# Kernel optimization log

Hardware: AMD Instinct MI355X
Metric: run time of the kernel (lower is better)

## Reference

```python
import math
import jax, jax.numpy as jnp
import numpy as np

B, S, D, H = 2, 2048, 2048, 16  # batch, seq, d_model, n_heads


def setup_inputs() -> dict:
    key = jax.random.key(0)
    ks = jax.random.split(key, 5)
    w_scale = 1.0 / math.sqrt(D)
    return {
        "x": jax.random.normal(ks[0], (B, S, D), jnp.float32),
        "attn_bias": jax.random.normal(ks[1], (1, H, S, S), jnp.float32) * 0.1,
        "Wqkv_w": jax.random.normal(ks[2], (3 * D, D), jnp.float32) * w_scale,
        "Wqkv_b": jnp.zeros((3 * D,), jnp.float32),
        "out_w": jax.random.normal(ks[3], (D, D), jnp.float32) * w_scale,
        "out_b": jnp.zeros((D,), jnp.float32),
    }


def reference(x, attn_bias, Wqkv_w, Wqkv_b, out_w, out_b):
    b, s, d = x.shape
    hd = d // H                      # head dim = 128
    scale = 1.0 / math.sqrt(hd)      # module default: 1/sqrt(d_model // n_heads)

    # fused QKV projection
    qkv = x @ Wqkv_w.T + Wqkv_b                       # [b, s, 3d]
    q, k, v = jnp.split(qkv, 3, axis=2)               # each [b, s, d]
    q = q.reshape(b, s, H, hd).transpose(0, 2, 1, 3)  # [b, h, s, hd]
    k = k.reshape(b, s, H, hd).transpose(0, 2, 1, 3)
    v = v.reshape(b, s, H, hd).transpose(0, 2, 1, 3)

    # scaled scores + additive bias (bias sliced to trailing q/k lengths)
    scores = jnp.einsum('bhqd,bhkd->bhqk', q, k) * scale
    scores = scores + attn_bias[:, :, -s:, -s:]

    # causal mask, masked positions set to dtype min (matches masked_fill with finfo.min)
    causal = jnp.tril(jnp.ones((s, s), dtype=bool))   # True = keep
    min_val = jnp.finfo(scores.dtype).min
    scores = jnp.where(causal[None, None, :, :], scores, min_val)

    p = jax.nn.softmax(scores, axis=-1)               # [b, h, s, s]
    out = jnp.einsum('bhqk,bhkd->bhqd', p, v)         # [b, h, s, hd]
    out = out.transpose(0, 2, 1, 3).reshape(b, s, d)  # [b, s, d]

    return out @ out_w.T + out_b
```

## Files before the change

kernel.cpp:

```cpp
#include <hip/hip_runtime.h>
#include <hip/hip_bf16.h>
#include <stdint.h>

#define H_  16
#define S_  2048
#define D_  2048
#define HD_ 128

typedef __bf16 bf16x8 __attribute__((ext_vector_type(8)));
typedef short  s16x8  __attribute__((ext_vector_type(8)));
typedef float  f32x4  __attribute__((ext_vector_type(4)));
typedef unsigned short u16x4 __attribute__((ext_vector_type(4)));

__device__ __forceinline__ unsigned short f2bf(float f) {
    unsigned u = __builtin_bit_cast(unsigned, f);
    u += 0x7fffu + ((u >> 16) & 1u);
    return (unsigned short)(u >> 16);
}

__device__ __forceinline__ float bf2f(unsigned short u) {
    unsigned v = ((unsigned)u) << 16;
    return __builtin_bit_cast(float, v);
}

__device__ __forceinline__ bf16x8 ld_bf8(const unsigned short* p) {
    s16x8 r = *reinterpret_cast<const s16x8*>(p);
    return __builtin_bit_cast(bf16x8, r);
}

#define GLOAD_LDS16(gp, lp)                                                     \
    __builtin_amdgcn_global_load_lds(                                            \
        (const __attribute__((address_space(1))) void*)(gp),                     \
        (__attribute__((address_space(3))) void*)(lp), 16, 0, 0)

__global__ __launch_bounds__(256) void cast_f32_bf16(const float* __restrict__ in,
                                                     unsigned short* __restrict__ out,
                                                     int n) {
    int i = (blockIdx.x * 256 + threadIdx.x) * 4;
    if (i >= n) return;
    float4 v = *reinterpret_cast<const float4*>(in + i);
    u16x4 o;
    o[0] = f2bf(v.x); o[1] = f2bf(v.y); o[2] = f2bf(v.z); o[3] = f2bf(v.w);
    *reinterpret_cast<u16x4*>(out + i) = o;
}

__global__ __launch_bounds__(256) void gemm_bt_qkv(const unsigned short* __restrict__ A,
                                                   const unsigned short* __restrict__ W,
                                                   const float* __restrict__ bias,
                                                   unsigned short* __restrict__ Qo,
                                                   unsigned short* __restrict__ Ko,
                                                   unsigned short* __restrict__ Vo) {
    __shared__ alignas(16) unsigned short As[128 * 32];
    __shared__ alignas(16) unsigned short Bs[128 * 32];
    const int t  = threadIdx.x;
    const int l  = t & 63, w = t >> 6;
    const int wr = w >> 1, wc = w & 1;
    const int lr = l & 15, g = l >> 4;

    const int GX = 48, NWG = 1536, CPX = NWG / 8;
    const int raw = blockIdx.y * GX + blockIdx.x;
    const int swz = (raw & 7) * CPX + (raw >> 3);
    const int m0 = (swz / GX) * 128, n0 = (swz % GX) * 128;
    const int Kd = D_;

    f32x4 zero = {0.f, 0.f, 0.f, 0.f};
    f32x4 acc[4][4];
    for (int i = 0; i < 4; ++i)
        for (int j = 0; j < 4; ++j) acc[i][j] = zero;

    const int ea = t * 8;
    const int rowA = ea >> 5, colA = ea & 31;

    for (int kt = 0; kt < Kd; kt += 32) {
        GLOAD_LDS16(A + (size_t)(m0 + rowA) * Kd + kt + colA, &As[ea]);
        GLOAD_LDS16(A + (size_t)(m0 + 64 + rowA) * Kd + kt + colA, &As[2048 + ea]);
        GLOAD_LDS16(W + (size_t)(n0 + rowA) * Kd + kt + colA, &Bs[ea]);
        GLOAD_LDS16(W + (size_t)(n0 + 64 + rowA) * Kd + kt + colA, &Bs[2048 + ea]);
        __syncthreads();
        bf16x8 af[4], bfr[4];
        for (int mi = 0; mi < 4; ++mi) af[mi]  = ld_bf8(&As[(wr * 64 + mi * 16 + lr) * 32 + g * 8]);
        for (int ni = 0; ni < 4; ++ni) bfr[ni] = ld_bf8(&Bs[(wc * 64 + ni * 16 + lr) * 32 + g * 8]);
        for (int mi = 0; mi < 4; ++mi)
            for (int ni = 0; ni < 4; ++ni)
                acc[mi][ni] = __builtin_amdgcn_mfma_f32_16x16x32_bf16(af[mi], bfr[ni], acc[mi][ni], 0, 0, 0);
        __syncthreads();
    }

    for (int mi = 0; mi < 4; ++mi) {
        for (int ni = 0; ni < 4; ++ni) {
            for (int i = 0; i < 4; ++i) {
                int m = m0 + wr * 64 + mi * 16 + g * 4 + i;
                int n = n0 + wc * 64 + ni * 16 + lr;
                float v = acc[mi][ni][i] + bias[n];
                int which = n >> 11;
                int n2 = n & 2047;
                int h = n2 >> 7, d = n2 & 127;
                int b = m >> 11, s = m & 2047;
                size_t idx = (((size_t)(b * H_ + h)) * S_ + s) * HD_ + d;
                unsigned short bv = f2bf(v);
                if (which == 0)      Qo[idx] = bv;
                else if (which == 1) Ko[idx] = bv;
                else                 Vo[idx] = bv;
            }
        }
    }
}

__global__ void transpose_v(const unsigned short* __restrict__ V,
                            unsigned short* __restrict__ Vt) {
    __shared__ alignas(16) unsigned short tile[32][33];
    const int bh = blockIdx.z;
    const int d0 = blockIdx.x * 32, s0 = blockIdx.y * 32;
    const int tx = threadIdx.x, ty = threadIdx.y;
    for (int r = 0; r < 4; ++r) {
        int s = s0 + ty + r * 8;
        tile[ty + r * 8][tx] = V[((size_t)bh * S_ + s) * HD_ + d0 + tx];
    }
    __syncthreads();
    for (int r = 0; r < 4; ++r) {
        int d = d0 + ty + r * 8;
        Vt[((size_t)bh * HD_ + d) * S_ + s0 + tx] = tile[tx][ty + r * 8];
    }
}

__global__ __launch_bounds__(256) void attn_kernel8(const unsigned short* __restrict__ Q,
                                                    const unsigned short* __restrict__ K,
                                                    const unsigned short* __restrict__ Vt,
                                                    const float* __restrict__ biasPtr,
                                                    unsigned short* __restrict__ O) {
    __shared__ alignas(16) unsigned short Klds[2][8192];
    __shared__ alignas(16) unsigned short Vlds[2][8192];
    __shared__ alignas(16) unsigned short Pbuf[4][16 * 64];

    const int t  = threadIdx.x;
    const int l  = t & 63, w = t >> 6;
    const int lr = l & 15, g = l >> 4;

    const int raw   = blockIdx.x;
    const int xcd   = raw & 7;
    const int local = raw >> 3;
    const int cu    = local & 31;
    const int slot  = local >> 5;
    const int qt    = (slot & 1) ? cu : (31 - cu);
    const int bh    = xcd + 8 * slot;
    const int b     = bh >> 4, head = bh & 15;

    const unsigned short* Qb = Q + (size_t)bh * S_ * HD_;
    const unsigned short* Kb = K + (size_t)bh * S_ * HD_;
    const unsigned short* Vb = Vt + (size_t)bh * HD_ * S_;
    const float* Bh32 = biasPtr + (size_t)head * S_ * S_;
    const float scale = 0.08838834764831845f;

    const int q0 = qt * 64 + w * 16;

    bf16x8 qf[4];
#pragma unroll
    for (int dc = 0; dc < 4; ++dc)
        qf[dc] = ld_bf8(Qb + (size_t)(q0 + lr) * HD_ + dc * 32 + g * 8);

    f32x4 zero = {0.f, 0.f, 0.f, 0.f};
    f32x4 o[8];
#pragma unroll
    for (int nc = 0; nc < 8; ++nc) o[nc] = zero;
    float lp[4] = {0.f, 0.f, 0.f, 0.f};

    unsigned short* Pw = Pbuf[w];

    auto STAGE = [&](int buf, int k0) {
#pragma unroll
        for (int p = 0; p < 4; ++p) {
            int lin = p * 4096 + t * 16;
            int row = lin >> 8;
            int colb = lin & 255;
            int scolb = colb ^ ((row & 7) << 4);
            GLOAD_LDS16(Kb + (size_t)(k0 + row) * HD_ + (scolb >> 1), &Klds[buf][lin >> 1]);
        }
#pragma unroll
        for (int p = 0; p < 4; ++p) {
            int lin = p * 4096 + t * 16;
            int row = lin >> 7;
            int colb = lin & 127;
            int scolb = colb ^ ((row & 7) << 4);
            GLOAD_LDS16(Vb + (size_t)row * S_ + k0 + (scolb >> 1), &Vlds[buf][lin >> 1]);
        }
    };

    STAGE(0, 0);
    __syncthreads();

    int cur = 0;
    for (int c = 0; c <= qt; ++c) {
        const int k0 = c * 64;

        if (c < qt) STAGE(cur ^ 1, k0 + 64);

        float bias_r[4][4];
#pragma unroll
        for (int i = 0; i < 4; ++i) {
            const int boff = (q0 + g * 4 + i) * S_ + k0 + lr;
#pragma unroll
            for (int kc = 0; kc < 4; ++kc)
                bias_r[i][kc] = Bh32[boff + kc * 16];
        }

        f32x4 s[4];
#pragma unroll
        for (int kc = 0; kc < 4; ++kc) s[kc] = zero;
#pragma unroll
        for (int kc = 0; kc < 4; ++kc) {
            bf16x8 kf[4];
#pragma unroll
            for (int dc = 0; dc < 4; ++dc)
                kf[dc] = ld_bf8(&Klds[cur][(kc * 16 + lr) * 128 + ((dc * 32 + g * 8) ^ ((lr & 7) << 3))]);
#pragma unroll
            for (int dc = 0; dc < 4; ++dc)
                s[kc] = __builtin_amdgcn_mfma_f32_16x16x32_bf16(qf[dc], kf[dc], s[kc], 0, 0, 0);
        }

        const bool lastc = (c == qt);
#pragma unroll
        for (int i = 0; i < 4; ++i) {
            const int rl   = w * 16 + g * 4 + i;
            const int prow = g * 4 + i;
            float e[4];
#pragma unroll
            for (int kc = 0; kc < 4; ++kc) {
                float v = s[kc][i] * scale + bias_r[i][kc];
                if (lastc && (kc * 16 + lr > rl)) v = -1.0e30f;
                e[kc] = __expf(v - 16.0f);
            }
            lp[i] += (e[0] + e[1]) + (e[2] + e[3]);
            const int sw = (prow & 7) << 3;
            Pw[(prow * 64 + 0  + lr) ^ sw] = f2bf(e[0]);
            Pw[(prow * 64 + 16 + lr) ^ sw] = f2bf(e[1]);
            Pw[(prow * 64 + 32 + lr) ^ sw] = f2bf(e[2]);
            Pw[(prow * 64 + 48 + lr) ^ sw] = f2bf(e[3]);
        }

#pragma unroll
        for (int kc2 = 0; kc2 < 2; ++kc2) {
            bf16x8 pa = ld_bf8(&Pw[(lr * 64 + kc2 * 32 + g * 8) ^ ((lr & 7) << 3)]);
#pragma unroll
            for (int nc = 0; nc < 8; ++nc) {
                bf16x8 vf = ld_bf8(&Vlds[cur][(nc * 16 + lr) * 64 + ((kc2 * 32 + g * 8) ^ ((lr & 7) << 3))]);
                o[nc] = __builtin_amdgcn_mfma_f32_16x16x32_bf16(pa, vf, o[nc], 0, 0, 0);
            }
        }

        __syncthreads();
        cur ^= 1;
    }

#pragma unroll
    for (int i = 0; i < 4; ++i) {
        lp[i] += __shfl_xor(lp[i], 1);
        lp[i] += __shfl_xor(lp[i], 2);
        lp[i] += __shfl_xor(lp[i], 4);
        lp[i] += __shfl_xor(lp[i], 8);
    }

#pragma unroll
    for (int i = 0; i < 4; ++i) {
        float inv = 1.0f / lp[i];
        int row = q0 + g * 4 + i;
#pragma unroll
        for (int nc = 0; nc < 8; ++nc) {
            O[((size_t)(b * S_ + row)) * D_ + head * HD_ + nc * 16 + lr] = f2bf(o[nc][i] * inv);
        }
    }
}

__global__ __launch_bounds__(256) void gemm_bt_out(const unsigned short* __restrict__ A,
                                                   const unsigned short* __restrict__ W,
                                                   const float* __restrict__ bias,
                                                   float* __restrict__ out) {
    __shared__ alignas(16) unsigned short As[128 * 32];
    __shared__ alignas(16) unsigned short Bs[128 * 32];
    const int t  = threadIdx.x;
    const int l  = t & 63, w = t >> 6;
    const int wr = w >> 1, wc = w & 1;
    const int lr = l & 15, g = l >> 4;

    const int GX = 16, NWG = 512, CPX = NWG / 8;
    const int raw = blockIdx.y * GX + blockIdx.x;
    const int swz = (raw & 7) * CPX + (raw >> 3);
    const int m0 = (swz / GX) * 128, n0 = (swz % GX) * 128;
    const int Kd = D_;

    f32x4 zero = {0.f, 0.f, 0.f, 0.f};
    f32x4 acc[4][4];
    for (int i = 0; i < 4; ++i)
        for (int j = 0; j < 4; ++j) acc[i][j] = zero;

    const int ea = t * 8;
    const int rowA = ea >> 5, colA = ea & 31;

    for (int kt = 0; kt < Kd; kt += 32) {
        GLOAD_LDS16(A + (size_t)(m0 + rowA) * Kd + kt + colA, &As[ea]);
        GLOAD_LDS16(A + (size_t)(m0 + 64 + rowA) * Kd + kt + colA, &As[2048 + ea]);
        GLOAD_LDS16(W + (size_t)(n0 + rowA) * Kd + kt + colA, &Bs[ea]);
        GLOAD_LDS16(W + (size_t)(n0 + 64 + rowA) * Kd + kt + colA, &Bs[2048 + ea]);
        __syncthreads();
        bf16x8 af[4], bfr[4];
        for (int mi = 0; mi < 4; ++mi) af[mi]  = ld_bf8(&As[(wr * 64 + mi * 16 + lr) * 32 + g * 8]);
        for (int ni = 0; ni < 4; ++ni) bfr[ni] = ld_bf8(&Bs[(wc * 64 + ni * 16 + lr) * 32 + g * 8]);
        for (int mi = 0; mi < 4; ++mi)
            for (int ni = 0; ni < 4; ++ni)
                acc[mi][ni] = __builtin_amdgcn_mfma_f32_16x16x32_bf16(af[mi], bfr[ni], acc[mi][ni], 0, 0, 0);
        __syncthreads();
    }

    for (int mi = 0; mi < 4; ++mi) {
        for (int ni = 0; ni < 4; ++ni) {
            for (int i = 0; i < 4; ++i) {
                int m = m0 + wr * 64 + mi * 16 + g * 4 + i;
                int n = n0 + wc * 64 + ni * 16 + lr;
                out[(size_t)m * D_ + n] = acc[mi][ni][i] + bias[n];
            }
        }
    }
}

extern "C" void kernel_launch(void* const* d_in, const int* in_sizes, int n_in,
                              void* d_out, int out_size, void* d_ws, size_t ws_size,
                              hipStream_t stream) {
    (void)in_sizes; (void)n_in; (void)out_size; (void)ws_size;
    const float* x         = (const float*)d_in[0];
    const float* attn_bias = (const float*)d_in[1];
    const float* Wqkv_w    = (const float*)d_in[2];
    const float* Wqkv_b    = (const float*)d_in[3];
    const float* out_w     = (const float*)d_in[4];
    const float* out_b     = (const float*)d_in[5];
    float* out = (float*)d_out;

    char* ws = (char*)d_ws;
    unsigned short* xb    = (unsigned short*)(ws);
    unsigned short* wqkvb = (unsigned short*)(ws + 16777216);
    unsigned short* woutb = (unsigned short*)(ws + 41943040);
    unsigned short* Qb    = (unsigned short*)(ws + 50331648);
    unsigned short* Kb    = (unsigned short*)(ws + 67108864);
    unsigned short* Vb    = (unsigned short*)(ws + 83886080);
    unsigned short* Vtb   = wqkvb;
    unsigned short* Ob    = xb;

    cast_f32_bf16<<<8192, 256, 0, stream>>>(x, xb, 8388608);
    cast_f32_bf16<<<12288, 256, 0, stream>>>(Wqkv_w, wqkvb, 12582912);
    cast_f32_bf16<<<4096, 256, 0, stream>>>(out_w, woutb, 4194304);
    gemm_bt_qkv<<<dim3(48, 32), 256, 0, stream>>>(xb, wqkvb, Wqkv_b, Qb, Kb, Vb);
    transpose_v<<<dim3(4, 64, 32), dim3(32, 8), 0, stream>>>(Vb, Vtb);
    attn_kernel8<<<1024, 256, 0, stream>>>(Qb, Kb, Vtb, attn_bias, Ob);
    gemm_bt_out<<<dim3(16, 32), 256, 0, stream>>>(Ob, woutb, out_b, out);
}
```

Measured before the change: 329.8 us.

## Double attention query tile per wave and write V transposed from QKV GEMM

The attention kernel now handles 128 query rows per block (32 per wave, two 16-row MFMA tiles), so each staged K/V chunk in LDS serves twice as many queries, and the grid drops to 512 blocks. The QKV GEMM epilogue writes V directly in head-dim-major layout, which removes the separate transpose kernel and its launch. The cost is more accumulator registers, which may lower occupancy, and fewer blocks for load balancing across causal tiles. The V stores become strided, so the GEMM epilogue writes are less coalesced.

```diff
diff --git a/kernel.cpp b/kernel.cpp
--- a/kernel.cpp
+++ b/kernel.cpp
@@ -16,11 +16,6 @@
     unsigned u = __builtin_bit_cast(unsigned, f);
     u += 0x7fffu + ((u >> 16) & 1u);
     return (unsigned short)(u >> 16);
-}
-
-__device__ __forceinline__ float bf2f(unsigned short u) {
-    unsigned v = ((unsigned)u) << 16;
-    return __builtin_bit_cast(float, v);
 }
 
 __device__ __forceinline__ bf16x8 ld_bf8(const unsigned short* p) {
@@ -96,41 +91,26 @@
                 int n2 = n & 2047;
                 int h = n2 >> 7, d = n2 & 127;
                 int b = m >> 11, s = m & 2047;
-                size_t idx = (((size_t)(b * H_ + h)) * S_ + s) * HD_ + d;
                 unsigned short bv = f2bf(v);
-                if (which == 0)      Qo[idx] = bv;
-                else if (which == 1) Ko[idx] = bv;
-                else                 Vo[idx] = bv;
-            }
-        }
-    }
-}
-
-__global__ void transpose_v(const unsigned short* __restrict__ V,
-                            unsigned short* __restrict__ Vt) {
-    __shared__ alignas(16) unsigned short tile[32][33];
-    const int bh = blockIdx.z;
-    const int d0 = blockIdx.x * 32, s0 = blockIdx.y * 32;
-    const int tx = threadIdx.x, ty = threadIdx.y;
-    for (int r = 0; r < 4; ++r) {
-        int s = s0 + ty + r * 8;
-        tile[ty + r * 8][tx] = V[((size_t)bh * S_ + s) * HD_ + d0 + tx];
-    }
-    __syncthreads();
-    for (int r = 0; r < 4; ++r) {
-        int d = d0 + ty + r * 8;
-        Vt[((size_t)bh * HD_ + d) * S_ + s0 + tx] = tile[tx][ty + r * 8];
-    }
-}
-
-__global__ __launch_bounds__(256) void attn_kernel8(const unsigned short* __restrict__ Q,
+                if (which == 0)
+                    Qo[(((size_t)(b * H_ + h)) * S_ + s) * HD_ + d] = bv;
+                else if (which == 1)
+                    Ko[(((size_t)(b * H_ + h)) * S_ + s) * HD_ + d] = bv;
+                else
+                    Vo[(((size_t)(b * H_ + h)) * HD_ + d) * S_ + s] = bv;
+            }
+        }
+    }
+}
+
+__global__ __launch_bounds__(256) void attn_kernel9(const unsigned short* __restrict__ Q,
                                                     const unsigned short* __restrict__ K,
                                                     const unsigned short* __restrict__ Vt,
                                                     const float* __restrict__ biasPtr,
                                                     unsigned short* __restrict__ O) {
     __shared__ alignas(16) unsigned short Klds[2][8192];
     __shared__ alignas(16) unsigned short Vlds[2][8192];
-    __shared__ alignas(16) unsigned short Pbuf[4][16 * 64];
+    __shared__ alignas(16) unsigned short Pbuf[4][32 * 64];
 
     const int t  = threadIdx.x;
     const int l  = t & 63, w = t >> 6;
@@ -139,10 +119,10 @@
     const int raw   = blockIdx.x;
     const int xcd   = raw & 7;
     const int local = raw >> 3;
+    const int group = local >> 5;
     const int cu    = local & 31;
-    const int slot  = local >> 5;
-    const int qt    = (slot & 1) ? cu : (31 - cu);
-    const int bh    = xcd + 8 * slot;
+    const int qt    = group ? (cu & 15) : (15 - (cu & 15));
+    const int bh    = xcd + 8 * ((cu >> 4) + 2 * group);
     const int b     = bh >> 4, head = bh & 15;
 
     const unsigned short* Qb = Q + (size_t)bh * S_ * HD_;
@@ -151,18 +131,20 @@
     const float* Bh32 = biasPtr + (size_t)head * S_ * S_;
     const float scale = 0.08838834764831845f;
 
-    const int q0 = qt * 64 + w * 16;
-
-    bf16x8 qf[4];
-#pragma unroll
-    for (int dc = 0; dc < 4; ++dc)
-        qf[dc] = ld_bf8(Qb + (size_t)(q0 + lr) * HD_ + dc * 32 + g * 8);
+    const int q0 = qt * 128 + w * 32;
+
+    bf16x8 qf[2][4];
+#pragma unroll
+    for (int m = 0; m < 2; ++m)
+#pragma unroll
+        for (int dc = 0; dc < 4; ++dc)
+            qf[m][dc] = ld_bf8(Qb + (size_t)(q0 + m * 16 + lr) * HD_ + dc * 32 + g * 8);
 
     f32x4 zero = {0.f, 0.f, 0.f, 0.f};
-    f32x4 o[8];
-#pragma unroll
-    for (int nc = 0; nc < 8; ++nc) o[nc] = zero;
-    float lp[4] = {0.f, 0.f, 0.f, 0.f};
+    f32x4 o0[8], o1[8];
+#pragma unroll
+    for (int nc = 0; nc < 8; ++nc) { o0[nc] = zero; o1[nc] = zero; }
+    float lp[2][4] = {{0.f, 0.f, 0.f, 0.f}, {0.f, 0.f, 0.f, 0.f}};
 
     unsigned short* Pw = Pbuf[w];
 
@@ -188,24 +170,27 @@
     STAGE(0, 0);
     __syncthreads();
 
+    const int nch = 2 * qt + 2;
     int cur = 0;
-    for (int c = 0; c <= qt; ++c) {
+    for (int c = 0; c < nch; ++c) {
         const int k0 = c * 64;
 
-        if (c < qt) STAGE(cur ^ 1, k0 + 64);
-
-        float bias_r[4][4];
-#pragma unroll
-        for (int i = 0; i < 4; ++i) {
-            const int boff = (q0 + g * 4 + i) * S_ + k0 + lr;
-#pragma unroll
-            for (int kc = 0; kc < 4; ++kc)
-                bias_r[i][kc] = Bh32[boff + kc * 16];
-        }
-
-        f32x4 s[4];
-#pragma unroll
-        for (int kc = 0; kc < 4; ++kc) s[kc] = zero;
+        if (c + 1 < nch) STAGE(cur ^ 1, k0 + 64);
+
+        float bias_r[2][4][4];
+#pragma unroll
+        for (int m = 0; m < 2; ++m)
+#pragma unroll
+            for (int i = 0; i < 4; ++i) {
+                const int boff = (q0 + m * 16 + g * 4 + i) * S_ + k0 + lr;
+#pragma unroll
+                for (int kc = 0; kc < 4; ++kc)
+                    bias_r[m][i][kc] = Bh32[boff + kc * 16];
+            }
+
+        f32x4 s0[4], s1[4];
+#pragma unroll
+        for (int kc = 0; kc < 4; ++kc) { s0[kc] = zero; s1[kc] = zero; }
 #pragma unroll
         for (int kc = 0; kc < 4; ++kc) {
             bf16x8 kf[4];
@@ -213,37 +198,45 @@
             for (int dc = 0; dc < 4; ++dc)
                 kf[dc] = ld_bf8(&Klds[cur][(kc * 16 + lr) * 128 + ((dc * 32 + g * 8) ^ ((lr & 7) << 3))]);
 #pragma unroll
-            for (int dc = 0; dc < 4; ++dc)
-                s[kc] = __builtin_amdgcn_mfma_f32_16x16x32_bf16(qf[dc], kf[dc], s[kc], 0, 0, 0);
-        }
-
-        const bool lastc = (c == qt);
-#pragma unroll
-        for (int i = 0; i < 4; ++i) {
-            const int rl   = w * 16 + g * 4 + i;
-            const int prow = g * 4 + i;
-            float e[4];
-#pragma unroll
-            for (int kc = 0; kc < 4; ++kc) {
-                float v = s[kc][i] * scale + bias_r[i][kc];
-                if (lastc && (kc * 16 + lr > rl)) v = -1.0e30f;
-                e[kc] = __expf(v - 16.0f);
-            }
-            lp[i] += (e[0] + e[1]) + (e[2] + e[3]);
-            const int sw = (prow & 7) << 3;
-            Pw[(prow * 64 + 0  + lr) ^ sw] = f2bf(e[0]);
-            Pw[(prow * 64 + 16 + lr) ^ sw] = f2bf(e[1]);
-            Pw[(prow * 64 + 32 + lr) ^ sw] = f2bf(e[2]);
-            Pw[(prow * 64 + 48 + lr) ^ sw] = f2bf(e[3]);
+            for (int dc = 0; dc < 4; ++dc) {
+                s0[kc] = __builtin_amdgcn_mfma_f32_16x16x32_bf16(qf[0][dc], kf[dc], s0[kc], 0, 0, 0);
+                s1[kc] = __builtin_amdgcn_mfma_f32_16x16x32_bf16(qf[1][dc], kf[dc], s1[kc], 0, 0, 0);
+            }
+        }
+
+        const bool maskzone = (c >= nch - 2);
+#pragma unroll
+        for (int m = 0; m < 2; ++m) {
+#pragma unroll
+            for (int i = 0; i < 4; ++i) {
+                const int rowabs = q0 + m * 16 + g * 4 + i;
+                const int prow   = m * 16 + g * 4 + i;
+                float e[4];
+#pragma unroll
+                for (int kc = 0; kc < 4; ++kc) {
+                    float sv = (m == 0) ? s0[kc][i] : s1[kc][i];
+                    float v = sv * scale + bias_r[m][i][kc];
+                    if (maskzone && (k0 + kc * 16 + lr > rowabs)) v = -1.0e30f;
+                    e[kc] = __expf(v - 16.0f);
+                }
+                lp[m][i] += (e[0] + e[1]) + (e[2] + e[3]);
+                const int sw = (prow & 7) << 3;
+                Pw[(prow * 64 + 0  + lr) ^ sw] = f2bf(e[0]);
+                Pw[(prow * 64 + 16 + lr) ^ sw] = f2bf(e[1]);
+                Pw[(prow * 64 + 32 + lr) ^ sw] = f2bf(e[2]);
+                Pw[(prow * 64 + 48 + lr) ^ sw] = f2bf(e[3]);
+            }
         }
 
 #pragma unroll
         for (int kc2 = 0; kc2 < 2; ++kc2) {
-            bf16x8 pa = ld_bf8(&Pw[(lr * 64 + kc2 * 32 + g * 8) ^ ((lr & 7) << 3)]);
+            bf16x8 pa0 = ld_bf8(&Pw[((lr)      * 64 + ((kc2 * 32 + g * 8) ^ ((lr & 7) << 3)))]);
+            bf16x8 pa1 = ld_bf8(&Pw[((16 + lr) * 64 + ((kc2 * 32 + g * 8) ^ ((lr & 7) << 3)))]);
 #pragma unroll
             for (int nc = 0; nc < 8; ++nc) {
                 bf16x8 vf = ld_bf8(&Vlds[cur][(nc * 16 + lr) * 64 + ((kc2 * 32 + g * 8) ^ ((lr & 7) << 3))]);
-                o[nc] = __builtin_amdgcn_mfma_f32_16x16x32_bf16(pa, vf, o[nc], 0, 0, 0);
+                o0[nc] = __builtin_amdgcn_mfma_f32_16x16x32_bf16(pa0, vf, o0[nc], 0, 0, 0);
+                o1[nc] = __builtin_amdgcn_mfma_f32_16x16x32_bf16(pa1, vf, o1[nc], 0, 0, 0);
             }
         }
 
@@ -252,20 +245,26 @@
     }
 
 #pragma unroll
-    for (int i = 0; i < 4; ++i) {
-        lp[i] += __shfl_xor(lp[i], 1);
-        lp[i] += __shfl_xor(lp[i], 2);
-        lp[i] += __shfl_xor(lp[i], 4);
-        lp[i] += __shfl_xor(lp[i], 8);
-    }
-
-#pragma unroll
-    for (int i = 0; i < 4; ++i) {
-        float inv = 1.0f / lp[i];
-        int row = q0 + g * 4 + i;
-#pragma unroll
-        for (int nc = 0; nc < 8; ++nc) {
-            O[((size_t)(b * S_ + row)) * D_ + head * HD_ + nc * 16 + lr] = f2bf(o[nc][i] * inv);
+    for (int m = 0; m < 2; ++m)
+#pragma unroll
+        for (int i = 0; i < 4; ++i) {
+            lp[m][i] += __shfl_xor(lp[m][i], 1);
+            lp[m][i] += __shfl_xor(lp[m][i], 2);
+            lp[m][i] += __shfl_xor(lp[m][i], 4);
+            lp[m][i] += __shfl_xor(lp[m][i], 8);
+        }
+
+#pragma unroll
+    for (int m = 0; m < 2; ++m) {
+#pragma unroll
+        for (int i = 0; i < 4; ++i) {
+            float inv = 1.0f / lp[m][i];
+            int row = q0 + m * 16 + g * 4 + i;
+#pragma unroll
+            for (int nc = 0; nc < 8; ++nc) {
+                float ov = (m == 0) ? o0[nc][i] : o1[nc][i];
+                O[((size_t)(b * S_ + row)) * D_ + head * HD_ + nc * 16 + lr] = f2bf(ov * inv);
+            }
         }
     }
 }
@@ -339,15 +338,13 @@
     unsigned short* woutb = (unsigned short*)(ws + 41943040);
     unsigned short* Qb    = (unsigned short*)(ws + 50331648);
     unsigned short* Kb    = (unsigned short*)(ws + 67108864);
-    unsigned short* Vb    = (unsigned short*)(ws + 83886080);
-    unsigned short* Vtb   = wqkvb;
+    unsigned short* Vtb   = (unsigned short*)(ws + 83886080);
     unsigned short* Ob    = xb;
 
     cast_f32_bf16<<<8192, 256, 0, stream>>>(x, xb, 8388608);
     cast_f32_bf16<<<12288, 256, 0, stream>>>(Wqkv_w, wqkvb, 12582912);
     cast_f32_bf16<<<4096, 256, 0, stream>>>(out_w, woutb, 4194304);
-    gemm_bt_qkv<<<dim3(48, 32), 256, 0, stream>>>(xb, wqkvb, Wqkv_b, Qb, Kb, Vb);
-    transpose_v<<<dim3(4, 64, 32), dim3(32, 8), 0, stream>>>(Vb, Vtb);
-    attn_kernel8<<<1024, 256, 0, stream>>>(Qb, Kb, Vtb, attn_bias, Ob);
+    gemm_bt_qkv<<<dim3(48, 32), 256, 0, stream>>>(xb, wqkvb, Wqkv_b, Qb, Kb, Vtb);
+    attn_kernel9<<<512, 256, 0, stream>>>(Qb, Kb, Vtb, attn_bias, Ob);
     gemm_bt_out<<<dim3(16, 32), 256, 0, stream>>>(Ob, woutb, out_b, out);
 }
```

Result: slower. 368.0 us (+11.6%).

## Write V transposed from QKV GEMM and shrink attention key chunks to 32

Applied to the files above, without the earlier changes.

The QKV GEMM epilogue now writes V directly in [bh, d, s] layout, so the separate transpose kernel and its extra global round trip go away. The attention kernel processes 32-key chunks instead of 64, which halves the K/V/P LDS footprint and cuts the wasted masked work on the diagonal tile. The cost is twice as many loop iterations, each with its own barrier and pipeline step, and strided 2-byte global stores for V in the GEMM epilogue.

```diff
diff --git a/kernel.cpp b/kernel.cpp
--- a/kernel.cpp
+++ b/kernel.cpp
@@ -16,11 +16,6 @@
     unsigned u = __builtin_bit_cast(unsigned, f);
     u += 0x7fffu + ((u >> 16) & 1u);
     return (unsigned short)(u >> 16);
-}
-
-__device__ __forceinline__ float bf2f(unsigned short u) {
-    unsigned v = ((unsigned)u) << 16;
-    return __builtin_bit_cast(float, v);
 }
 
 __device__ __forceinline__ bf16x8 ld_bf8(const unsigned short* p) {
@@ -96,41 +91,26 @@
                 int n2 = n & 2047;
                 int h = n2 >> 7, d = n2 & 127;
                 int b = m >> 11, s = m & 2047;
-                size_t idx = (((size_t)(b * H_ + h)) * S_ + s) * HD_ + d;
                 unsigned short bv = f2bf(v);
-                if (which == 0)      Qo[idx] = bv;
-                else if (which == 1) Ko[idx] = bv;
-                else                 Vo[idx] = bv;
+                if (which == 0)
+                    Qo[(((size_t)(b * H_ + h)) * S_ + s) * HD_ + d] = bv;
+                else if (which == 1)
+                    Ko[(((size_t)(b * H_ + h)) * S_ + s) * HD_ + d] = bv;
+                else
+                    Vo[(((size_t)(b * H_ + h)) * HD_ + d) * S_ + s] = bv;
             }
         }
     }
 }
 
-__global__ void transpose_v(const unsigned short* __restrict__ V,
-                            unsigned short* __restrict__ Vt) {
-    __shared__ alignas(16) unsigned short tile[32][33];
-    const int bh = blockIdx.z;
-    const int d0 = blockIdx.x * 32, s0 = blockIdx.y * 32;
-    const int tx = threadIdx.x, ty = threadIdx.y;
-    for (int r = 0; r < 4; ++r) {
-        int s = s0 + ty + r * 8;
-        tile[ty + r * 8][tx] = V[((size_t)bh * S_ + s) * HD_ + d0 + tx];
-    }
-    __syncthreads();
-    for (int r = 0; r < 4; ++r) {
-        int d = d0 + ty + r * 8;
-        Vt[((size_t)bh * HD_ + d) * S_ + s0 + tx] = tile[tx][ty + r * 8];
-    }
-}
-
-__global__ __launch_bounds__(256) void attn_kernel8(const unsigned short* __restrict__ Q,
-                                                    const unsigned short* __restrict__ K,
-                                                    const unsigned short* __restrict__ Vt,
-                                                    const float* __restrict__ biasPtr,
-                                                    unsigned short* __restrict__ O) {
-    __shared__ alignas(16) unsigned short Klds[2][8192];
-    __shared__ alignas(16) unsigned short Vlds[2][8192];
-    __shared__ alignas(16) unsigned short Pbuf[4][16 * 64];
+__global__ __launch_bounds__(256) void attn_kernel10(const unsigned short* __restrict__ Q,
+                                                     const unsigned short* __restrict__ K,
+                                                     const unsigned short* __restrict__ Vt,
+                                                     const float* __restrict__ biasPtr,
+                                                     unsigned short* __restrict__ O) {
+    __shared__ alignas(16) unsigned short Klds[2][4096];
+    __shared__ alignas(16) unsigned short Vlds[2][4096];
+    __shared__ alignas(16) unsigned short Pbuf[4][16 * 32];
 
     const int t  = threadIdx.x;
     const int l  = t & 63, w = t >> 6;
@@ -168,7 +148,7 @@
 
     auto STAGE = [&](int buf, int k0) {
 #pragma unroll
-        for (int p = 0; p < 4; ++p) {
+        for (int p = 0; p < 2; ++p) {
             int lin = p * 4096 + t * 16;
             int row = lin >> 8;
             int colb = lin & 255;
@@ -176,11 +156,11 @@
             GLOAD_LDS16(Kb + (size_t)(k0 + row) * HD_ + (scolb >> 1), &Klds[buf][lin >> 1]);
         }
 #pragma unroll
-        for (int p = 0; p < 4; ++p) {
+        for (int p = 0; p < 2; ++p) {
             int lin = p * 4096 + t * 16;
-            int row = lin >> 7;
-            int colb = lin & 127;
-            int scolb = colb ^ ((row & 7) << 4);
+            int row = lin >> 6;
+            int colb = lin & 63;
+            int scolb = colb ^ ((row & 3) << 4);
             GLOAD_LDS16(Vb + (size_t)row * S_ + k0 + (scolb >> 1), &Vlds[buf][lin >> 1]);
         }
     };
@@ -188,26 +168,26 @@
     STAGE(0, 0);
     __syncthreads();
 
+    const int nch = 2 * qt + 2;
     int cur = 0;
-    for (int c = 0; c <= qt; ++c) {
-        const int k0 = c * 64;
-
-        if (c < qt) STAGE(cur ^ 1, k0 + 64);
-
-        float bias_r[4][4];
+    for (int c = 0; c < nch; ++c) {
+        const int k0 = c * 32;
+
+        if (c + 1 < nch) STAGE(cur ^ 1, k0 + 32);
+
+        float bias_r[4][2];
 #pragma unroll
         for (int i = 0; i < 4; ++i) {
             const int boff = (q0 + g * 4 + i) * S_ + k0 + lr;
 #pragma unroll
-            for (int kc = 0; kc < 4; ++kc)
+            for (int kc = 0; kc < 2; ++kc)
                 bias_r[i][kc] = Bh32[boff + kc * 16];
         }
 
-        f32x4 s[4];
-#pragma unroll
-        for (int kc = 0; kc < 4; ++kc) s[kc] = zero;
-#pragma unroll
-        for (int kc = 0; kc < 4; ++kc) {
+        f32x4 s[2];
+        s[0] = zero; s[1] = zero;
+#pragma unroll
+        for (int kc = 0; kc < 2; ++kc) {
             bf16x8 kf[4];
 #pragma unroll
             for (int dc = 0; dc < 4; ++dc)
@@ -217,32 +197,29 @@
                 s[kc] = __builtin_amdgcn_mfma_f32_16x16x32_bf16(qf[dc], kf[dc], s[kc], 0, 0, 0);
         }
 
-        const bool lastc = (c == qt);
+        const bool maskzone = (c >= nch - 2);
 #pragma unroll
         for (int i = 0; i < 4; ++i) {
-            const int rl   = w * 16 + g * 4 + i;
-            const int prow = g * 4 + i;
-            float e[4];
-#pragma unroll
-            for (int kc = 0; kc < 4; ++kc) {
+            const int rowabs = q0 + g * 4 + i;
+            const int prow   = g * 4 + i;
+            float e[2];
+#pragma unroll
+            for (int kc = 0; kc < 2; ++kc) {
                 float v = s[kc][i] * scale + bias_r[i][kc];
-                if (lastc && (kc * 16 + lr > rl)) v = -1.0e30f;
+                if (maskzone && (k0 + kc * 16 + lr > rowabs)) v = -1.0e30f;
                 e[kc] = __expf(v - 16.0f);
             }
-            lp[i] += (e[0] + e[1]) + (e[2] + e[3]);
-            const int sw = (prow & 7) << 3;
-            Pw[(prow * 64 + 0  + lr) ^ sw] = f2bf(e[0]);
-            Pw[(prow * 64 + 16 + lr) ^ sw] = f2bf(e[1]);
-            Pw[(prow * 64 + 32 + lr) ^ sw] = f2bf(e[2]);
-            Pw[(prow * 64 + 48 + lr) ^ sw] = f2bf(e[3]);
-        }
-
-#pragma unroll
-        for (int kc2 = 0; kc2 < 2; ++kc2) {
-            bf16x8 pa = ld_bf8(&Pw[(lr * 64 + kc2 * 32 + g * 8) ^ ((lr & 7) << 3)]);
+            lp[i] += e[0] + e[1];
+            const int sw = (prow & 3) << 3;
+            Pw[(prow * 32 + 0  + lr) ^ sw] = f2bf(e[0]);
+            Pw[(prow * 32 + 16 + lr) ^ sw] = f2bf(e[1]);
+        }
+
+        {
+            bf16x8 pa = ld_bf8(&Pw[lr * 32 + ((g * 8) ^ ((lr & 3) << 3))]);
 #pragma unroll
             for (int nc = 0; nc < 8; ++nc) {
-                bf16x8 vf = ld_bf8(&Vlds[cur][(nc * 16 + lr) * 64 + ((kc2 * 32 + g * 8) ^ ((lr & 7) << 3))]);
+                bf16x8 vf = ld_bf8(&Vlds[cur][(nc * 16 + lr) * 32 + ((g * 8) ^ ((lr & 3) << 3))]);
                 o[nc] = __builtin_amdgcn_mfma_f32_16x16x32_bf16(pa, vf, o[nc], 0, 0, 0);
             }
         }
@@ -339,15 +316,13 @@
     unsigned short* woutb = (unsigned short*)(ws + 41943040);
     unsigned short* Qb    = (unsigned short*)(ws + 50331648);
     unsigned short* Kb    = (unsigned short*)(ws + 67108864);
-    unsigned short* Vb    = (unsigned short*)(ws + 83886080);
-    unsigned short* Vtb   = wqkvb;
+    unsigned short* Vtb   = (unsigned short*)(ws + 83886080);
     unsigned short* Ob    = xb;
 
     cast_f32_bf16<<<8192, 256, 0, stream>>>(x, xb, 8388608);
     cast_f32_bf16<<<12288, 256, 0, stream>>>(Wqkv_w, wqkvb, 12582912);
     cast_f32_bf16<<<4096, 256, 0, stream>>>(out_w, woutb, 4194304);
-    gemm_bt_qkv<<<dim3(48, 32), 256, 0, stream>>>(xb, wqkvb, Wqkv_b, Qb, Kb, Vb);
-    transpose_v<<<dim3(4, 64, 32), dim3(32, 8), 0, stream>>>(Vb, Vtb);
-    attn_kernel8<<<1024, 256, 0, stream>>>(Qb, Kb, Vtb, attn_bias, Ob);
+    gemm_bt_qkv<<<dim3(48, 32), 256, 0, stream>>>(xb, wqkvb, Wqkv_b, Qb, Kb, Vtb);
+    attn_kernel10<<<1024, 256, 0, stream>>>(Qb, Kb, Vtb, attn_bias, Ob);
     gemm_bt_out<<<dim3(16, 32), 256, 0, stream>>>(Ob, woutb, out_b, out);
 }
```

Measured after the change: 325.2 us. Within noise of the previous version (-1.4%).
